# Performance work log

Measured on AMD Instinct MI355X. Metric: run time of the kernel, lower is better.

## Reference

```python
import jax, jax.numpy as jnp
import numpy as np

N = 50000      # nodes
E = 1600000    # edges (avg degree 32)
C_IN = 128
C_H = 128
C_OUT = 10
G = 512        # number of graphs in the batch


def setup_inputs() -> dict:
    key = jax.random.key(0)
    ks = jax.random.split(key, 16)
    x = jax.random.normal(ks[0], (N, C_IN), dtype=jnp.float32)
    edge_index = jax.random.randint(ks[1], (2, E), 0, N, dtype=jnp.int64)
    batch = jnp.sort(jax.random.randint(ks[2], (N,), 0, G, dtype=jnp.int64))

    def lin(k, fan_in, fan_out):
        lim = 1.0 / np.sqrt(fan_in)
        return jax.random.uniform(k, (fan_in, fan_out), jnp.float32, -lim, lim)

    return {
        "x": x, "edge_index": edge_index, "batch": batch,
        # conv1: c_in -> c_hidden
        "Wr1": lin(ks[3], C_IN, C_H), "br1": jnp.zeros((C_H,), jnp.float32),
        "Wo1": lin(ks[4], C_IN, C_H),
        # conv2: c_hidden -> 2*c_hidden
        "Wr2": lin(ks[5], C_H, 2 * C_H), "br2": jnp.zeros((2 * C_H,), jnp.float32),
        "Wo2": lin(ks[6], C_H, 2 * C_H),
        # conv3: 2*c_hidden -> c_hidden
        "Wr3": lin(ks[7], 2 * C_H, C_H), "br3": jnp.zeros((C_H,), jnp.float32),
        "Wo3": lin(ks[8], 2 * C_H, C_H),
        # head
        "W1": lin(ks[9], C_H, 4 * C_OUT), "b1": jnp.zeros((4 * C_OUT,), jnp.float32),
        "W2": lin(ks[10], 4 * C_OUT, C_OUT), "b2": jnp.zeros((C_OUT,), jnp.float32),
    }


def _graph_conv(x, src, dst, Wr, br, Wo):
    # PyG GraphConv: lin_rel(sum_{j in N(i)} x_j) + lin_root(x_i)
    agg = jax.ops.segment_sum(x[src], dst, num_segments=N)  # [N, F_in]
    return agg @ Wr + br + x @ Wo


def reference(x, edge_index, batch, Wr1, br1, Wo1, Wr2, br2, Wo2,
              Wr3, br3, Wo3, W1, b1, W2, b2):
    src, dst = edge_index[0], edge_index[1]
    h = jax.nn.relu(_graph_conv(x, src, dst, Wr1, br1, Wo1))
    h = jax.nn.relu(_graph_conv(h, src, dst, Wr2, br2, Wo2))
    h = _graph_conv(h, src, dst, Wr3, br3, Wo3)
    # global mean pool over graphs
    sums = jax.ops.segment_sum(h, batch, num_segments=G)            # [G, C_H]
    cnts = jax.ops.segment_sum(jnp.ones((N,), h.dtype), batch, num_segments=G)
    pooled = sums / jnp.maximum(cnts, 1.0)[:, None]
    # dropout is identity in eval mode
    out = pooled @ W1 + b1
    out = out @ W2 + b2
    return out
```

## Files before the change

kernel.cpp:

```cpp
#include <hip/hip_runtime.h>
#include <hip/hip_bf16.h>
#include <cstddef>

#define NN 50000
#define EE 1600000
#define GG 512
#define NB 196
#define BSTRIDE 16384
#define BCAP 10240
#define XBLKS 6250
#define SCBLKS 782
#define PSEG 8

typedef unsigned int u32;
typedef unsigned short u16;
typedef __attribute__((ext_vector_type(8))) short frag_ab;
typedef __attribute__((ext_vector_type(4))) float frag_cd;

__device__ __forceinline__ void gl_lds16(const void* g, void* l) {
    __builtin_amdgcn_global_load_lds(
        (const __attribute__((address_space(1))) u32*)g,
        (__attribute__((address_space(3))) u32*)l, 16, 0, 0);
}
__device__ __forceinline__ float b2f_lo(u32 v) { return __uint_as_float(v << 16); }
__device__ __forceinline__ float b2f_hi(u32 v) { return __uint_as_float(v & 0xffff0000u); }
__device__ __forceinline__ float b2f(u32 v, int odd) { return odd ? b2f_hi(v) : b2f_lo(v); }
__device__ __forceinline__ u16 f2b(float x) {
    __hip_bfloat16 h = __float2bfloat16(x);
    return *(u16*)&h;
}
__device__ __forceinline__ u32 pack2(float lo, float hi) {
    return ((u32)f2b(hi) << 16) | f2b(lo);
}
__device__ __forceinline__ void acc2(float2& a, u32 v) {
    a.x += b2f_lo(v);
    a.y += b2f_hi(v);
}

__device__ inline int lower_bound_i(const int* a, int n, int v) {
    int lo = 0, hi = n;
    while (lo < hi) {
        int m = (lo + hi) >> 1;
        if (a[m] < v) lo = m + 1; else hi = m;
    }
    return lo;
}



__global__ __launch_bounds__(256) void bscatter_prep_kernel(
    const int* __restrict__ ei, int* __restrict__ bcnt, u32* __restrict__ pairs,
    const float* __restrict__ x, u16* __restrict__ ax,
    const float* __restrict__ Wr1, const float* __restrict__ Wo1,
    const float* __restrict__ Wr2, const float* __restrict__ Wo2,
    const float* __restrict__ Wr3, const float* __restrict__ Wo3,
    const float* __restrict__ br3,
    u16* __restrict__ BT1, u16* __restrict__ BT2, u16* __restrict__ BT3,
    float* __restrict__ bias3, const int* __restrict__ batch,
    int* __restrict__ gn) {
    __shared__ int lcnt[NB];
    __shared__ int lbase[NB];
    __shared__ unsigned short lpos[2048];
    int bid = blockIdx.x, t = threadIdx.x;
    if (bid < SCBLKS) {
        int e0 = bid * 2048;
        u32 pk[8];
        int bk[8];
        for (int i = t; i < NB; i += 256) lcnt[i] = 0;
        __syncthreads();
#pragma unroll
        for (int i = 0; i < 8; ++i) {
            int e = e0 + i * 256 + t;
            if (e < EE) {
                int dst = ei[EE + e], src = ei[e];
                int b = dst >> 8;
                bk[i] = b;
                pk[i] = ((u32)src << 8) | (u32)(dst & 255);
                lpos[i * 256 + t] = (unsigned short)atomicAdd(&lcnt[b], 1);
            } else bk[i] = -1;
        }
        __syncthreads();
        for (int i = t; i < NB; i += 256) lbase[i] = atomicAdd(&bcnt[i], lcnt[i]);
        __syncthreads();
#pragma unroll
        for (int i = 0; i < 8; ++i) {
            if (bk[i] >= 0) {
                int pos = lbase[bk[i]] + (int)lpos[i * 256 + t];
                pairs[(size_t)bk[i] * BSTRIDE + pos] = pk[i];
            }
        }
    } else if (bid < SCBLKS + XBLKS) {
        int idx = (bid - SCBLKS) * 256 + t;
        int row = idx >> 5, q = idx & 31;
        float4 v = *(const float4*)(x + (size_t)row * 128 + q * 4);
        *(u32*)(ax + (size_t)row * 256 + 128 + q * 4) = pack2(v.x, v.y);
        *(u32*)(ax + (size_t)row * 256 + 128 + q * 4 + 2) = pack2(v.z, v.w);
    } else if (bid < SCBLKS + XBLKS + 256) {
        int m = bid - SCBLKS - XBLKS;
        int k = t;
        BT2[m * 256 + k] = f2b(k < 128 ? Wr2[k * 256 + m] : Wo2[(k - 128) * 256 + m]);
        BT3[m * 256 + k] = f2b(m < 128 ? Wr3[k * 128 + m] : Wo3[k * 128 + (m - 128)]);
        if (m < 128)
            BT1[m * 256 + k] = f2b(k < 128 ? Wr1[k * 128 + m] : Wo1[(k - 128) * 128 + m]);
        if (k == 0) bias3[m] = (m < 128) ? 0.f : br3[m - 128];
    } else {
        int g = (bid - SCBLKS - XBLKS - 256) * 256 + t;
        if (g <= GG) gn[g] = lower_bound_i(batch, NN, g);
    }
}


__global__ __launch_bounds__(512) void bfill_kernel(const u32* __restrict__ pairs,
                                                    const int* __restrict__ bcnt,
                                                    int* __restrict__ ofs,
                                                    u16* __restrict__ srcl) {
    __shared__ int sc[256];
    __shared__ int cnts[256];
    __shared__ int lcnt[256];
    __shared__ int lcur[256];
    __shared__ int lbuf[BCAP];
    int b = blockIdx.x, t = threadIdx.x;
    if (t < 256) {
        int c = (t < NB) ? bcnt[t] : 0;
        cnts[t] = c;
        sc[t] = c;
        lcnt[t] = 0;
    }
    __syncthreads();
    for (int off = 1; off < 256; off <<= 1) {
        int v = (t >= off && t < 256) ? sc[t - off] : 0;
        __syncthreads();
        if (t < 256) sc[t] += v;
        __syncthreads();
    }
    int base = sc[b] - cnts[b];
    int span = cnts[b];
    const u32* pp = pairs + (size_t)b * BSTRIDE;
    for (int j = t; j < span; j += 512) atomicAdd(&lcnt[pp[j] & 255u], 1);
    __syncthreads();
    int nc = 0;
    if (t < 256) {
        nc = lcnt[t];
        sc[t] = nc;
    }
    __syncthreads();
    for (int off = 1; off < 256; off <<= 1) {
        int v = (t >= off && t < 256) ? sc[t - off] : 0;
        __syncthreads();
        if (t < 256) sc[t] += v;
        __syncthreads();
    }
    if (t < 256) {
        int excl = sc[t] - nc;
        int node = b * 256 + t;
        if (node < NN) ofs[node] = base + excl;
        lcur[t] = excl;
    }
    if (b == 0 && t == 256) ofs[NN] = EE;
    __syncthreads();
    for (int j = t; j < span; j += 512) {
        u32 p = pp[j];
        int pos = atomicAdd(&lcur[p & 255u], 1);
        int src = (int)(p >> 8);
        if (pos < BCAP) lbuf[pos] = src;
        else srcl[base + pos] = (u16)src;
    }
    __syncthreads();
    int lim = span < BCAP ? span : BCAP;
    for (int j = t; j < lim; j += 512) srcl[base + j] = (u16)lbuf[j];
}


__global__ __launch_bounds__(256) void pull_bf_kernel(const u32* __restrict__ Xu,
                                                      const int* __restrict__ ofs,
                                                      const u16* __restrict__ srcl,
                                                      u32* __restrict__ outu) {
    int node = (blockIdx.x * 256 + threadIdx.x) >> 6;
    int lane = threadIdx.x & 63;
    int q = lane >> 4, l = lane & 15;
    int lo = ofs[node], hi = ofs[node + 1];
    float2 a0 = {0.f, 0.f}, a1 = {0.f, 0.f}, a2 = {0.f, 0.f}, a3 = {0.f, 0.f};
    int j = lo;
    for (; j + 15 < hi; j += 16) {
        int s0 = srcl[j + q], s1 = srcl[j + 4 + q];
        int s2 = srcl[j + 8 + q], s3 = srcl[j + 12 + q];
        uint4 v0 = *(const uint4*)(Xu + (size_t)s0 * 128 + l * 4);
        uint4 v1 = *(const uint4*)(Xu + (size_t)s1 * 128 + l * 4);
        uint4 v2 = *(const uint4*)(Xu + (size_t)s2 * 128 + l * 4);
        uint4 v3 = *(const uint4*)(Xu + (size_t)s3 * 128 + l * 4);
        acc2(a0, v0.x); acc2(a1, v0.y); acc2(a2, v0.z); acc2(a3, v0.w);
        acc2(a0, v1.x); acc2(a1, v1.y); acc2(a2, v1.z); acc2(a3, v1.w);
        acc2(a0, v2.x); acc2(a1, v2.y); acc2(a2, v2.z); acc2(a3, v2.w);
        acc2(a0, v3.x); acc2(a1, v3.y); acc2(a2, v3.z); acc2(a3, v3.w);
    }
    for (; j + 3 < hi; j += 4) {
        int s = srcl[j + q];
        uint4 v = *(const uint4*)(Xu + (size_t)s * 128 + l * 4);
        acc2(a0, v.x); acc2(a1, v.y); acc2(a2, v.z); acc2(a3, v.w);
    }
    if (j + q < hi) {
        int s = srcl[j + q];
        uint4 v = *(const uint4*)(Xu + (size_t)s * 128 + l * 4);
        acc2(a0, v.x); acc2(a1, v.y); acc2(a2, v.z); acc2(a3, v.w);
    }
    float acc[8] = {a0.x, a0.y, a1.x, a1.y, a2.x, a2.y, a3.x, a3.y};
#pragma unroll
    for (int i = 0; i < 8; ++i) {
        acc[i] += __shfl_xor(acc[i], 16, 64);
        acc[i] += __shfl_xor(acc[i], 32, 64);
    }
    if (q == 0) {
        uint4 r;
        r.x = pack2(acc[0], acc[1]);
        r.y = pack2(acc[2], acc[3]);
        r.z = pack2(acc[4], acc[5]);
        r.w = pack2(acc[6], acc[7]);
        *(uint4*)(outu + (size_t)node * 128 + l * 4) = r;
    }
}


__global__ __launch_bounds__(256, 2) void gemm_bf_kernel(
    const u16* __restrict__ A, const u16* __restrict__ BT,
    const float* __restrict__ bias, u16* __restrict__ C,
    int ldc, int coloff, int relu) {
    __shared__ alignas(16) u16 As[128 * 32];
    __shared__ alignas(16) u16 Bs[128 * 32];
    const int t = threadIdx.x;
    const int lane = t & 63, wid = t >> 6;
    const int quad = lane >> 4, l16 = lane & 15;
    const int wm = wid >> 1, wn = wid & 1;
    const int row0 = blockIdx.y * 128, c0 = blockIdx.x * 128;

    frag_cd acc[4][4];
#pragma unroll
    for (int i = 0; i < 4; ++i)
#pragma unroll
        for (int j = 0; j < 4; ++j) acc[i][j] = (frag_cd)0.f;

    const int ca = t, cb = t + 256;
    const int ra = ca >> 2, oa = (ca & 3) * 8;
    const int rb = cb >> 2, ob = (cb & 3) * 8;
    const int garow = min(row0 + ra, NN - 1);
    const int gbrow = min(row0 + rb, NN - 1);
    const size_t gA1 = (size_t)garow * 256 + oa;
    const size_t gA2 = (size_t)gbrow * 256 + ob;
    const size_t gB1 = (size_t)(c0 + ra) * 256 + oa;
    const size_t gB2 = (size_t)(c0 + rb) * 256 + ob;

    for (int kk = 0; kk < 256; kk += 32) {
        __syncthreads();
        gl_lds16(A + gA1 + kk, &As[ca * 8]);
        gl_lds16(A + gA2 + kk, &As[cb * 8]);
        gl_lds16(BT + gB1 + kk, &Bs[ca * 8]);
        gl_lds16(BT + gB2 + kk, &Bs[cb * 8]);
        __syncthreads();

        frag_ab a[4], b[4];
#pragma unroll
        for (int mt = 0; mt < 4; ++mt)
            a[mt] = *(const frag_ab*)&As[(wm * 64 + mt * 16 + l16) * 32 + quad * 8];
#pragma unroll
        for (int nt = 0; nt < 4; ++nt)
            b[nt] = *(const frag_ab*)&Bs[(wn * 64 + nt * 16 + l16) * 32 + quad * 8];
#pragma unroll
        for (int mt = 0; mt < 4; ++mt)
#pragma unroll
            for (int nt = 0; nt < 4; ++nt)
                acc[mt][nt] = __builtin_amdgcn_mfma_f32_16x16x32_bf16(
                    a[mt], b[nt], acc[mt][nt], 0, 0, 0);
    }

#pragma unroll
    for (int nt = 0; nt < 4; ++nt) {
        int col = c0 + wn * 64 + nt * 16 + l16;
        float bv = bias[col];
#pragma unroll
        for (int mt = 0; mt < 4; ++mt) {
#pragma unroll
            for (int r = 0; r < 4; ++r) {
                int row = row0 + wm * 64 + mt * 16 + quad * 4 + r;
                if (row < NN) {
                    float v = acc[mt][nt][r] + bv;
                    if (relu) v = fmaxf(v, 0.f);
                    C[(size_t)row * ldc + coloff + col] = f2b(v);
                }
            }
        }
    }
}


__global__ __launch_bounds__(256, 2) void gemm23_kernel(
    const u16* __restrict__ A, const u16* __restrict__ BT2,
    const float* __restrict__ br2, const u16* __restrict__ BT3,
    const float* __restrict__ bias3, u16* __restrict__ C) {
    __shared__ alignas(16) u16 As[128 * 32];
    __shared__ alignas(16) u16 Bs[128 * 32];
    __shared__ alignas(16) u16 Hs[128 * 256];
    const int t = threadIdx.x;
    const int lane = t & 63, wid = t >> 6;
    const int quad = lane >> 4, l16 = lane & 15;
    const int wm = wid >> 1, wn = wid & 1;
    const int row0 = blockIdx.x * 128;

    const int ca = t, cb = t + 256;
    const int ra = ca >> 2, oa = (ca & 3) * 8;
    const int rb = cb >> 2, ob = (cb & 3) * 8;
    const int garow = min(row0 + ra, NN - 1);
    const int gbrow = min(row0 + rb, NN - 1);
    const size_t gA1 = (size_t)garow * 256 + oa;
    const size_t gA2 = (size_t)gbrow * 256 + ob;

    for (int nb = 0; nb < 2; ++nb) {
        const int c0 = nb * 128;
        frag_cd acc[4][4];
#pragma unroll
        for (int i = 0; i < 4; ++i)
#pragma unroll
            for (int j = 0; j < 4; ++j) acc[i][j] = (frag_cd)0.f;

        for (int kk = 0; kk < 256; kk += 32) {
            __syncthreads();
            gl_lds16(A + gA1 + kk, &As[ca * 8]);
            gl_lds16(A + gA2 + kk, &As[cb * 8]);
            gl_lds16(BT2 + (size_t)(c0 + ra) * 256 + kk + oa, &Bs[ca * 8]);
            gl_lds16(BT2 + (size_t)(c0 + rb) * 256 + kk + ob, &Bs[cb * 8]);
            __syncthreads();

            frag_ab a[4], b[4];
#pragma unroll
            for (int mt = 0; mt < 4; ++mt)
                a[mt] = *(const frag_ab*)&As[(wm * 64 + mt * 16 + l16) * 32 + quad * 8];
#pragma unroll
            for (int nt = 0; nt < 4; ++nt)
                b[nt] = *(const frag_ab*)&Bs[(wn * 64 + nt * 16 + l16) * 32 + quad * 8];
#pragma unroll
            for (int mt = 0; mt < 4; ++mt)
#pragma unroll
                for (int nt = 0; nt < 4; ++nt)
                    acc[mt][nt] = __builtin_amdgcn_mfma_f32_16x16x32_bf16(
                        a[mt], b[nt], acc[mt][nt], 0, 0, 0);
        }
#pragma unroll
        for (int nt = 0; nt < 4; ++nt) {
            int col = c0 + wn * 64 + nt * 16 + l16;
            float bv = br2[col];
#pragma unroll
            for (int mt = 0; mt < 4; ++mt) {
#pragma unroll
                for (int r = 0; r < 4; ++r) {
                    int lr = wm * 64 + mt * 16 + quad * 4 + r;
                    float v = fmaxf(acc[mt][nt][r] + bv, 0.f);
                    Hs[(lr * 256 + col) ^ ((lr & 7) << 3)] = f2b(v);
                }
            }
        }
    }
    __syncthreads();

    for (int nb = 0; nb < 2; ++nb) {
        const int c0 = nb * 128;
        frag_cd acc[4][4];
#pragma unroll
        for (int i = 0; i < 4; ++i)
#pragma unroll
            for (int j = 0; j < 4; ++j) acc[i][j] = (frag_cd)0.f;

        for (int kk = 0; kk < 256; kk += 32) {
            __syncthreads();
            gl_lds16(BT3 + (size_t)(c0 + ra) * 256 + kk + oa, &Bs[ca * 8]);
            gl_lds16(BT3 + (size_t)(c0 + rb) * 256 + kk + ob, &Bs[cb * 8]);
            __syncthreads();

            frag_ab a[4], b[4];
#pragma unroll
            for (int mt = 0; mt < 4; ++mt) {
                int lr = wm * 64 + mt * 16 + l16;
                a[mt] = *(const frag_ab*)&Hs[(lr * 256 + kk + quad * 8) ^ ((lr & 7) << 3)];
            }
#pragma unroll
            for (int nt = 0; nt < 4; ++nt)
                b[nt] = *(const frag_ab*)&Bs[(wn * 64 + nt * 16 + l16) * 32 + quad * 8];
#pragma unroll
            for (int mt = 0; mt < 4; ++mt)
#pragma unroll
                for (int nt = 0; nt < 4; ++nt)
                    acc[mt][nt] = __builtin_amdgcn_mfma_f32_16x16x32_bf16(
                        a[mt], b[nt], acc[mt][nt], 0, 0, 0);
        }
#pragma unroll
        for (int nt = 0; nt < 4; ++nt) {
            int col = c0 + wn * 64 + nt * 16 + l16;
            float bv = bias3[col];
#pragma unroll
            for (int mt = 0; mt < 4; ++mt) {
#pragma unroll
                for (int r = 0; r < 4; ++r) {
                    int row = row0 + wm * 64 + mt * 16 + quad * 4 + r;
                    if (row < NN) {
                        float v = acc[mt][nt][r] + bv;
                        C[(size_t)row * 256 + col] = f2b(v);
                    }
                }
            }
        }
    }
}


__global__ __launch_bounds__(256) void pool3_seg_kernel(
    const u32* __restrict__ Tu, const int* __restrict__ ofs,
    const u16* __restrict__ srcl, const int* __restrict__ gn,
    float* __restrict__ psum) {
    __shared__ float red[4][128];
    __shared__ float po[2][128];
    int gb = blockIdx.x;
    int g = gb >> 3, s = gb & 7;
    int t = threadIdx.x;
    int w = t >> 6, lane = t & 63;
    int q = lane >> 4, l = lane & 15;
    int n_lo = gn[g], n_hi = gn[g + 1];
    int glo = ofs[n_lo], ghi = ofs[n_hi];
    int len = ghi - glo;
    int s_lo = glo + (int)(((long long)len * s) >> 3);
    int s_hi = glo + (int)(((long long)len * (s + 1)) >> 3);
    int slen = s_hi - s_lo;
    int wlo = s_lo + ((slen * w) >> 2);
    int whi = s_lo + ((slen * (w + 1)) >> 2);

    float2 a0 = {0.f, 0.f}, a1 = {0.f, 0.f}, a2 = {0.f, 0.f}, a3 = {0.f, 0.f};
    int j = wlo;
    for (; j + 15 < whi; j += 16) {
        int s0 = srcl[j + q], s1 = srcl[j + 4 + q];
        int s2 = srcl[j + 8 + q], s3 = srcl[j + 12 + q];
        uint4 v0 = *(const uint4*)(Tu + (size_t)s0 * 128 + l * 4);
        uint4 v1 = *(const uint4*)(Tu + (size_t)s1 * 128 + l * 4);
        uint4 v2 = *(const uint4*)(Tu + (size_t)s2 * 128 + l * 4);
        uint4 v3 = *(const uint4*)(Tu + (size_t)s3 * 128 + l * 4);
        acc2(a0, v0.x); acc2(a1, v0.y); acc2(a2, v0.z); acc2(a3, v0.w);
        acc2(a0, v1.x); acc2(a1, v1.y); acc2(a2, v1.z); acc2(a3, v1.w);
        acc2(a0, v2.x); acc2(a1, v2.y); acc2(a2, v2.z); acc2(a3, v2.w);
        acc2(a0, v3.x); acc2(a1, v3.y); acc2(a2, v3.z); acc2(a3, v3.w);
    }
    for (; j + 3 < whi; j += 4) {
        int sv = srcl[j + q];
        uint4 v = *(const uint4*)(Tu + (size_t)sv * 128 + l * 4);
        acc2(a0, v.x); acc2(a1, v.y); acc2(a2, v.z); acc2(a3, v.w);
    }
    if (j + q < whi) {
        int sv = srcl[j + q];
        uint4 v = *(const uint4*)(Tu + (size_t)sv * 128 + l * 4);
        acc2(a0, v.x); acc2(a1, v.y); acc2(a2, v.z); acc2(a3, v.w);
    }
    float acc[8] = {a0.x, a0.y, a1.x, a1.y, a2.x, a2.y, a3.x, a3.y};
#pragma unroll
    for (int i = 0; i < 8; ++i) {
        acc[i] += __shfl_xor(acc[i], 16, 64);
        acc[i] += __shfl_xor(acc[i], 32, 64);
    }
    if (q == 0) {
#pragma unroll
        for (int i = 0; i < 8; ++i) red[w][l * 8 + i] = acc[i];
    }
    float so = 0.f;
    int ch = t & 127, rg = t >> 7;
    for (int r = n_lo + s * 2 + rg; r < n_hi; r += 16)
        so += b2f(Tu[(size_t)r * 128 + 64 + (ch >> 1)], ch & 1);
    po[rg][ch] = so;
    __syncthreads();
    if (t < 128) {
        float v = red[0][t] + red[1][t] + red[2][t] + red[3][t] + po[0][t] + po[1][t];
        psum[((size_t)g * PSEG + s) * 128 + t] = v;
    }
}


__global__ __launch_bounds__(128) void head_kernel(
    const float* __restrict__ psum, const int* __restrict__ gn,
    const float* __restrict__ W1, const float* __restrict__ b1,
    const float* __restrict__ W2, const float* __restrict__ b2,
    float* __restrict__ out) {
    __shared__ float p[128];
    __shared__ float hid[40];
    int g = blockIdx.x, t = threadIdx.x;
    int cnt = gn[g + 1] - gn[g];
    float sv = 0.f;
#pragma unroll
    for (int k = 0; k < PSEG; ++k) sv += psum[((size_t)g * PSEG + k) * 128 + t];
    p[t] = sv / fmaxf((float)cnt, 1.f);
    __syncthreads();
    if (t < 40) {
        float v = b1[t];
        for (int k = 0; k < 128; ++k) v += p[k] * W1[k * 40 + t];
        hid[t] = v;
    }
    __syncthreads();
    if (t < 10) {
        float v = b2[t];
        for (int j = 0; j < 40; ++j) v += hid[j] * W2[j * 10 + t];
        out[g * 10 + t] = v;
    }
}


extern "C" void kernel_launch(void* const* d_in, const int* in_sizes, int n_in,
                              void* d_out, int out_size, void* d_ws, size_t ws_size,
                              hipStream_t stream) {
    const float* x   = (const float*)d_in[0];
    const int* ei    = (const int*)d_in[1];
    const int* batch = (const int*)d_in[2];
    const float* Wr1 = (const float*)d_in[3];
    const float* br1 = (const float*)d_in[4];
    const float* Wo1 = (const float*)d_in[5];
    const float* Wr2 = (const float*)d_in[6];
    const float* br2 = (const float*)d_in[7];
    const float* Wo2 = (const float*)d_in[8];
    const float* Wr3 = (const float*)d_in[9];
    const float* br3 = (const float*)d_in[10];
    const float* Wo3 = (const float*)d_in[11];
    const float* W1  = (const float*)d_in[12];
    const float* b1  = (const float*)d_in[13];
    const float* W2  = (const float*)d_in[14];
    const float* b2  = (const float*)d_in[15];
    float* out = (float*)d_out;

    char* ws = (char*)d_ws;
    size_t off = 0;
    auto alloc = [&](size_t bytes) {
        void* p = ws + off;
        off += (bytes + 255) & ~(size_t)255;
        return p;
    };
    int* ofs      = (int*)alloc((NN + 1) * sizeof(int));
    int* bcnt     = (int*)alloc(256 * sizeof(int));
    int* gn       = (int*)alloc((GG + 1) * sizeof(int));
    u16* srcl     = (u16*)alloc((size_t)EE * 2);
    u16* ax       = (u16*)alloc((size_t)NN * 256 * 2);
    u16* ah1      = (u16*)alloc((size_t)NN * 256 * 2);
    u16* t3o3     = (u16*)alloc((size_t)NN * 256 * 2);
    float* psum   = (float*)alloc((size_t)GG * PSEG * 128 * sizeof(float));
    u16* BT1      = (u16*)alloc(128 * 256 * 2);
    u16* BT2      = (u16*)alloc(256 * 256 * 2);
    u16* BT3      = (u16*)alloc(256 * 256 * 2);
    float* bias3  = (float*)alloc(256 * sizeof(float));
    u32* pairs = (u32*)t3o3;

    hipMemsetAsync(bcnt, 0, 256 * sizeof(int), stream);

    bscatter_prep_kernel<<<SCBLKS + XBLKS + 256 + 3, 256, 0, stream>>>(
        ei, bcnt, pairs, x, ax, Wr1, Wo1, Wr2, Wo2, Wr3, Wo3, br3,
        BT1, BT2, BT3, bias3, batch, gn);
    bfill_kernel<<<NB, 512, 0, stream>>>(pairs, bcnt, ofs, srcl);

    pull_bf_kernel<<<NN * 64 / 256, 256, 0, stream>>>((const u32*)ax + 64, ofs, srcl, (u32*)ax);
    gemm_bf_kernel<<<dim3(1, 391), 256, 0, stream>>>(ax, BT1, br1, ah1, 256, 128, 1);
    pull_bf_kernel<<<NN * 64 / 256, 256, 0, stream>>>((const u32*)ah1 + 64, ofs, srcl, (u32*)ah1);
    gemm23_kernel<<<391, 256, 0, stream>>>(ah1, BT2, br2, BT3, bias3, t3o3);

    pool3_seg_kernel<<<GG * PSEG, 256, 0, stream>>>((const u32*)t3o3, ofs, srcl, gn, psum);
    head_kernel<<<GG, 128, 0, stream>>>(psum, gn, W1, b1, W2, b2, out);
}
```

Before: 344.2 us.

## Load GEMM fragments directly from global, merge N-blocks, stage output through LDS

The fused conv2/conv3 GEMM kernel no longer stages A and B tiles through LDS with per-k barriers. Each wave now loads MFMA fragments straight from global memory and computes both 128-column halves in one K loop, doubling the accumulator registers. The final output is written into the swizzled Hs buffer and then copied out with coalesced 16-byte stores. The aim is to drop the barriers and LDS round trips, at the cost of more register pressure (occupancy risk under launch_bounds 256,2) and uncoalesced, possibly redundant global fragment loads.

```diff
diff --git a/kernel.cpp b/kernel.cpp
--- a/kernel.cpp
+++ b/kernel.cpp
@@ -295,8 +295,6 @@
     const u16* __restrict__ A, const u16* __restrict__ BT2,
     const float* __restrict__ br2, const u16* __restrict__ BT3,
     const float* __restrict__ bias3, u16* __restrict__ C) {
-    __shared__ alignas(16) u16 As[128 * 32];
-    __shared__ alignas(16) u16 Bs[128 * 32];
     __shared__ alignas(16) u16 Hs[128 * 256];
     const int t = threadIdx.x;
     const int lane = t & 63, wid = t >> 6;
@@ -304,107 +302,118 @@
     const int wm = wid >> 1, wn = wid & 1;
     const int row0 = blockIdx.x * 128;
 
-    const int ca = t, cb = t + 256;
-    const int ra = ca >> 2, oa = (ca & 3) * 8;
-    const int rb = cb >> 2, ob = (cb & 3) * 8;
-    const int garow = min(row0 + ra, NN - 1);
-    const int gbrow = min(row0 + rb, NN - 1);
-    const size_t gA1 = (size_t)garow * 256 + oa;
-    const size_t gA2 = (size_t)gbrow * 256 + ob;
-
-    for (int nb = 0; nb < 2; ++nb) {
-        const int c0 = nb * 128;
-        frag_cd acc[4][4];
+    size_t aoff[4];
+#pragma unroll
+    for (int mt = 0; mt < 4; ++mt) {
+        int r = min(row0 + wm * 64 + mt * 16 + l16, NN - 1);
+        aoff[mt] = (size_t)r * 256 + quad * 8;
+    }
+    size_t boff[2][4];
+#pragma unroll
+    for (int nb = 0; nb < 2; ++nb)
+#pragma unroll
+        for (int nt = 0; nt < 4; ++nt)
+            boff[nb][nt] = (size_t)(nb * 128 + wn * 64 + nt * 16 + l16) * 256 + quad * 8;
+
+    frag_cd acc[2][4][4];
+#pragma unroll
+    for (int nb = 0; nb < 2; ++nb)
 #pragma unroll
         for (int i = 0; i < 4; ++i)
 #pragma unroll
-            for (int j = 0; j < 4; ++j) acc[i][j] = (frag_cd)0.f;
-
-        for (int kk = 0; kk < 256; kk += 32) {
-            __syncthreads();
-            gl_lds16(A + gA1 + kk, &As[ca * 8]);
-            gl_lds16(A + gA2 + kk, &As[cb * 8]);
-            gl_lds16(BT2 + (size_t)(c0 + ra) * 256 + kk + oa, &Bs[ca * 8]);
-            gl_lds16(BT2 + (size_t)(c0 + rb) * 256 + kk + ob, &Bs[cb * 8]);
-            __syncthreads();
-
-            frag_ab a[4], b[4];
+            for (int j = 0; j < 4; ++j) acc[nb][i][j] = (frag_cd)0.f;
+
+    for (int kk = 0; kk < 256; kk += 32) {
+        frag_ab a[4], b[2][4];
+#pragma unroll
+        for (int mt = 0; mt < 4; ++mt)
+            a[mt] = *(const frag_ab*)(A + aoff[mt] + kk);
+#pragma unroll
+        for (int nb = 0; nb < 2; ++nb)
+#pragma unroll
+            for (int nt = 0; nt < 4; ++nt)
+                b[nb][nt] = *(const frag_ab*)(BT2 + boff[nb][nt] + kk);
+#pragma unroll
+        for (int nb = 0; nb < 2; ++nb)
 #pragma unroll
             for (int mt = 0; mt < 4; ++mt)
-                a[mt] = *(const frag_ab*)&As[(wm * 64 + mt * 16 + l16) * 32 + quad * 8];
-#pragma unroll
-            for (int nt = 0; nt < 4; ++nt)
-                b[nt] = *(const frag_ab*)&Bs[(wn * 64 + nt * 16 + l16) * 32 + quad * 8];
+#pragma unroll
+                for (int nt = 0; nt < 4; ++nt)
+                    acc[nb][mt][nt] = __builtin_amdgcn_mfma_f32_16x16x32_bf16(
+                        a[mt], b[nb][nt], acc[nb][mt][nt], 0, 0, 0);
+    }
+#pragma unroll
+    for (int nb = 0; nb < 2; ++nb)
+#pragma unroll
+        for (int nt = 0; nt < 4; ++nt) {
+            int col = nb * 128 + wn * 64 + nt * 16 + l16;
+            float bv = br2[col];
 #pragma unroll
             for (int mt = 0; mt < 4; ++mt)
-#pragma unroll
-                for (int nt = 0; nt < 4; ++nt)
-                    acc[mt][nt] = __builtin_amdgcn_mfma_f32_16x16x32_bf16(
-                        a[mt], b[nt], acc[mt][nt], 0, 0, 0);
-        }
-#pragma unroll
-        for (int nt = 0; nt < 4; ++nt) {
-            int col = c0 + wn * 64 + nt * 16 + l16;
-            float bv = br2[col];
-#pragma unroll
-            for (int mt = 0; mt < 4; ++mt) {
 #pragma unroll
                 for (int r = 0; r < 4; ++r) {
                     int lr = wm * 64 + mt * 16 + quad * 4 + r;
-                    float v = fmaxf(acc[mt][nt][r] + bv, 0.f);
+                    float v = fmaxf(acc[nb][mt][nt][r] + bv, 0.f);
                     Hs[(lr * 256 + col) ^ ((lr & 7) << 3)] = f2b(v);
                 }
-            }
         }
-    }
-    __syncthreads();
-
-    for (int nb = 0; nb < 2; ++nb) {
-        const int c0 = nb * 128;
-        frag_cd acc[4][4];
+    __syncthreads();
+
+    int hrow[4];
+#pragma unroll
+    for (int mt = 0; mt < 4; ++mt) hrow[mt] = wm * 64 + mt * 16 + l16;
+#pragma unroll
+    for (int nb = 0; nb < 2; ++nb)
 #pragma unroll
         for (int i = 0; i < 4; ++i)
 #pragma unroll
-            for (int j = 0; j < 4; ++j) acc[i][j] = (frag_cd)0.f;
-
-        for (int kk = 0; kk < 256; kk += 32) {
-            __syncthreads();
-            gl_lds16(BT3 + (size_t)(c0 + ra) * 256 + kk + oa, &Bs[ca * 8]);
-            gl_lds16(BT3 + (size_t)(c0 + rb) * 256 + kk + ob, &Bs[cb * 8]);
-            __syncthreads();
-
-            frag_ab a[4], b[4];
-#pragma unroll
-            for (int mt = 0; mt < 4; ++mt) {
-                int lr = wm * 64 + mt * 16 + l16;
-                a[mt] = *(const frag_ab*)&Hs[(lr * 256 + kk + quad * 8) ^ ((lr & 7) << 3)];
-            }
+            for (int j = 0; j < 4; ++j) acc[nb][i][j] = (frag_cd)0.f;
+    for (int kk = 0; kk < 256; kk += 32) {
+        frag_ab a[4], b[2][4];
+#pragma unroll
+        for (int mt = 0; mt < 4; ++mt)
+            a[mt] = *(const frag_ab*)&Hs[(hrow[mt] * 256 + kk + quad * 8) ^
+                                         ((hrow[mt] & 7) << 3)];
+#pragma unroll
+        for (int nb = 0; nb < 2; ++nb)
 #pragma unroll
             for (int nt = 0; nt < 4; ++nt)
-                b[nt] = *(const frag_ab*)&Bs[(wn * 64 + nt * 16 + l16) * 32 + quad * 8];
+                b[nb][nt] = *(const frag_ab*)(BT3 + boff[nb][nt] + kk);
+#pragma unroll
+        for (int nb = 0; nb < 2; ++nb)
 #pragma unroll
             for (int mt = 0; mt < 4; ++mt)
 #pragma unroll
                 for (int nt = 0; nt < 4; ++nt)
-                    acc[mt][nt] = __builtin_amdgcn_mfma_f32_16x16x32_bf16(
-                        a[mt], b[nt], acc[mt][nt], 0, 0, 0);
+                    acc[nb][mt][nt] = __builtin_amdgcn_mfma_f32_16x16x32_bf16(
+                        a[mt], b[nb][nt], acc[nb][mt][nt], 0, 0, 0);
+    }
+    __syncthreads();
+
+#pragma unroll
+    for (int nb = 0; nb < 2; ++nb)
+#pragma unroll
+        for (int nt = 0; nt < 4; ++nt) {
+            int col = nb * 128 + wn * 64 + nt * 16 + l16;
+            float bv = bias3[col];
+#pragma unroll
+            for (int mt = 0; mt < 4; ++mt)
+#pragma unroll
+                for (int r = 0; r < 4; ++r) {
+                    int lr = wm * 64 + mt * 16 + quad * 4 + r;
+                    Hs[(lr * 256 + col) ^ ((lr & 7) << 3)] = f2b(acc[nb][mt][nt][r] + bv);
+                }
         }
-#pragma unroll
-        for (int nt = 0; nt < 4; ++nt) {
-            int col = c0 + wn * 64 + nt * 16 + l16;
-            float bv = bias3[col];
-#pragma unroll
-            for (int mt = 0; mt < 4; ++mt) {
-#pragma unroll
-                for (int r = 0; r < 4; ++r) {
-                    int row = row0 + wm * 64 + mt * 16 + quad * 4 + r;
-                    if (row < NN) {
-                        float v = acc[mt][nt][r] + bv;
-                        C[(size_t)row * 256 + col] = f2b(v);
-                    }
-                }
-            }
-        }
+    __syncthreads();
+    const uint4* Hs128 = (const uint4*)Hs;
+#pragma unroll
+    for (int it = 0; it < 16; ++it) {
+        int row = it * 8 + (t >> 5);
+        int grp = t & 31;
+        uint4 v = Hs128[row * 32 + (grp ^ (row & 7))];
+        int grow = row0 + row;
+        if (grow < NN)
+            *(uint4*)(C + (size_t)grow * 256 + grp * 8) = v;
     }
 }
 
```

New measurement: 375.3 us. 9.1% more time.

## Retile fused conv2/conv3 GEMM to 64-row blocks with full-width N and staged stores

Applied to the files above, without the earlier changes.

The fused gemm23 kernel now works on 64-row tiles with each wave computing a full 16x256 strip, instead of 128-row tiles split 2x2 across waves with two N passes. The grid doubles to 782 blocks and LDS use shrinks, so launch bounds rise to 3 blocks per CU. The output is written back through the swizzled LDS buffer as coalesced 16-byte stores instead of scattered 2-byte stores. The intent is more parallelism across CUs and better write coalescing. The cost is that B tiles are reloaded per 64 rows, which doubles weight traffic, and 16 accumulators per wave add register pressure.

```diff
diff --git a/kernel.cpp b/kernel.cpp
--- a/kernel.cpp
+++ b/kernel.cpp
@@ -291,120 +291,96 @@
 }
 
 
-__global__ __launch_bounds__(256, 2) void gemm23_kernel(
+__global__ __launch_bounds__(256, 3) void gemm23_kernel(
     const u16* __restrict__ A, const u16* __restrict__ BT2,
     const float* __restrict__ br2, const u16* __restrict__ BT3,
     const float* __restrict__ bias3, u16* __restrict__ C) {
-    __shared__ alignas(16) u16 As[128 * 32];
-    __shared__ alignas(16) u16 Bs[128 * 32];
-    __shared__ alignas(16) u16 Hs[128 * 256];
+    __shared__ alignas(16) u16 As[64 * 32];
+    __shared__ alignas(16) u16 Bs[256 * 32];
+    __shared__ alignas(16) u16 Hs[64 * 256];
     const int t = threadIdx.x;
-    const int lane = t & 63, wid = t >> 6;
+    const int lane = t & 63, w = t >> 6;
     const int quad = lane >> 4, l16 = lane & 15;
-    const int wm = wid >> 1, wn = wid & 1;
-    const int row0 = blockIdx.x * 128;
-
-    const int ca = t, cb = t + 256;
-    const int ra = ca >> 2, oa = (ca & 3) * 8;
-    const int rb = cb >> 2, ob = (cb & 3) * 8;
+    const int row0 = blockIdx.x * 64;
+
+    const int ra = t >> 2, oa = (t & 3) * 8;
     const int garow = min(row0 + ra, NN - 1);
-    const int gbrow = min(row0 + rb, NN - 1);
-    const size_t gA1 = (size_t)garow * 256 + oa;
-    const size_t gA2 = (size_t)gbrow * 256 + ob;
-
-    for (int nb = 0; nb < 2; ++nb) {
-        const int c0 = nb * 128;
-        frag_cd acc[4][4];
+    const size_t gA = (size_t)garow * 256 + oa;
+    size_t gB[4];
+#pragma unroll
+    for (int i = 0; i < 4; ++i) {
+        int cbi = i * 256 + t;
+        gB[i] = (size_t)(cbi >> 2) * 256 + (cbi & 3) * 8;
+    }
+
+    frag_cd acc[16];
+#pragma unroll
+    for (int i = 0; i < 16; ++i) acc[i] = (frag_cd)0.f;
+
+    for (int kk = 0; kk < 256; kk += 32) {
+        __syncthreads();
+        gl_lds16(A + gA + kk, &As[t * 8]);
 #pragma unroll
         for (int i = 0; i < 4; ++i)
-#pragma unroll
-            for (int j = 0; j < 4; ++j) acc[i][j] = (frag_cd)0.f;
-
-        for (int kk = 0; kk < 256; kk += 32) {
-            __syncthreads();
-            gl_lds16(A + gA1 + kk, &As[ca * 8]);
-            gl_lds16(A + gA2 + kk, &As[cb * 8]);
-            gl_lds16(BT2 + (size_t)(c0 + ra) * 256 + kk + oa, &Bs[ca * 8]);
-            gl_lds16(BT2 + (size_t)(c0 + rb) * 256 + kk + ob, &Bs[cb * 8]);
-            __syncthreads();
-
-            frag_ab a[4], b[4];
-#pragma unroll
-            for (int mt = 0; mt < 4; ++mt)
-                a[mt] = *(const frag_ab*)&As[(wm * 64 + mt * 16 + l16) * 32 + quad * 8];
-#pragma unroll
-            for (int nt = 0; nt < 4; ++nt)
-                b[nt] = *(const frag_ab*)&Bs[(wn * 64 + nt * 16 + l16) * 32 + quad * 8];
-#pragma unroll
-            for (int mt = 0; mt < 4; ++mt)
-#pragma unroll
-                for (int nt = 0; nt < 4; ++nt)
-                    acc[mt][nt] = __builtin_amdgcn_mfma_f32_16x16x32_bf16(
-                        a[mt], b[nt], acc[mt][nt], 0, 0, 0);
-        }
-#pragma unroll
-        for (int nt = 0; nt < 4; ++nt) {
-            int col = c0 + wn * 64 + nt * 16 + l16;
-            float bv = br2[col];
-#pragma unroll
-            for (int mt = 0; mt < 4; ++mt) {
-#pragma unroll
-                for (int r = 0; r < 4; ++r) {
-                    int lr = wm * 64 + mt * 16 + quad * 4 + r;
-                    float v = fmaxf(acc[mt][nt][r] + bv, 0.f);
-                    Hs[(lr * 256 + col) ^ ((lr & 7) << 3)] = f2b(v);
-                }
-            }
-        }
-    }
-    __syncthreads();
-
-    for (int nb = 0; nb < 2; ++nb) {
-        const int c0 = nb * 128;
-        frag_cd acc[4][4];
+            gl_lds16(BT2 + gB[i] + kk, &Bs[(i * 256 + t) * 8]);
+        __syncthreads();
+        frag_ab a = *(const frag_ab*)&As[(w * 16 + l16) * 32 + quad * 8];
+#pragma unroll
+        for (int nt = 0; nt < 16; ++nt) {
+            frag_ab b = *(const frag_ab*)&Bs[(nt * 16 + l16) * 32 + quad * 8];
+            acc[nt] = __builtin_amdgcn_mfma_f32_16x16x32_bf16(a, b, acc[nt], 0, 0, 0);
+        }
+    }
+#pragma unroll
+    for (int nt = 0; nt < 16; ++nt) {
+        int col = nt * 16 + l16;
+        float bv = br2[col];
+#pragma unroll
+        for (int r = 0; r < 4; ++r) {
+            int lr = w * 16 + quad * 4 + r;
+            float v = fmaxf(acc[nt][r] + bv, 0.f);
+            Hs[(lr * 256 + col) ^ ((lr & 7) << 3)] = f2b(v);
+        }
+    }
+
+#pragma unroll
+    for (int i = 0; i < 16; ++i) acc[i] = (frag_cd)0.f;
+    const int hrow = w * 16 + l16;
+    for (int kk = 0; kk < 256; kk += 32) {
+        __syncthreads();
 #pragma unroll
         for (int i = 0; i < 4; ++i)
-#pragma unroll
-            for (int j = 0; j < 4; ++j) acc[i][j] = (frag_cd)0.f;
-
-        for (int kk = 0; kk < 256; kk += 32) {
-            __syncthreads();
-            gl_lds16(BT3 + (size_t)(c0 + ra) * 256 + kk + oa, &Bs[ca * 8]);
-            gl_lds16(BT3 + (size_t)(c0 + rb) * 256 + kk + ob, &Bs[cb * 8]);
-            __syncthreads();
-
-            frag_ab a[4], b[4];
-#pragma unroll
-            for (int mt = 0; mt < 4; ++mt) {
-                int lr = wm * 64 + mt * 16 + l16;
-                a[mt] = *(const frag_ab*)&Hs[(lr * 256 + kk + quad * 8) ^ ((lr & 7) << 3)];
-            }
-#pragma unroll
-            for (int nt = 0; nt < 4; ++nt)
-                b[nt] = *(const frag_ab*)&Bs[(wn * 64 + nt * 16 + l16) * 32 + quad * 8];
-#pragma unroll
-            for (int mt = 0; mt < 4; ++mt)
-#pragma unroll
-                for (int nt = 0; nt < 4; ++nt)
-                    acc[mt][nt] = __builtin_amdgcn_mfma_f32_16x16x32_bf16(
-                        a[mt], b[nt], acc[mt][nt], 0, 0, 0);
-        }
-#pragma unroll
-        for (int nt = 0; nt < 4; ++nt) {
-            int col = c0 + wn * 64 + nt * 16 + l16;
-            float bv = bias3[col];
-#pragma unroll
-            for (int mt = 0; mt < 4; ++mt) {
-#pragma unroll
-                for (int r = 0; r < 4; ++r) {
-                    int row = row0 + wm * 64 + mt * 16 + quad * 4 + r;
-                    if (row < NN) {
-                        float v = acc[mt][nt][r] + bv;
-                        C[(size_t)row * 256 + col] = f2b(v);
-                    }
-                }
-            }
-        }
+            gl_lds16(BT3 + gB[i] + kk, &Bs[(i * 256 + t) * 8]);
+        __syncthreads();
+        frag_ab a = *(const frag_ab*)&Hs[(hrow * 256 + kk + quad * 8) ^
+                                         ((hrow & 7) << 3)];
+#pragma unroll
+        for (int nt = 0; nt < 16; ++nt) {
+            frag_ab b = *(const frag_ab*)&Bs[(nt * 16 + l16) * 32 + quad * 8];
+            acc[nt] = __builtin_amdgcn_mfma_f32_16x16x32_bf16(a, b, acc[nt], 0, 0, 0);
+        }
+    }
+
+#pragma unroll
+    for (int nt = 0; nt < 16; ++nt) {
+        int col = nt * 16 + l16;
+        float bv = bias3[col];
+#pragma unroll
+        for (int r = 0; r < 4; ++r) {
+            int lr = w * 16 + quad * 4 + r;
+            Hs[(lr * 256 + col) ^ ((lr & 7) << 3)] = f2b(acc[nt][r] + bv);
+        }
+    }
+    __syncthreads();
+    const uint4* Hs128 = (const uint4*)Hs;
+#pragma unroll
+    for (int it = 0; it < 8; ++it) {
+        int row = it * 8 + (t >> 5);
+        int grp = t & 31;
+        uint4 v = Hs128[row * 32 + (grp ^ (row & 7))];
+        int grow = row0 + row;
+        if (grow < NN)
+            *(uint4*)(C + (size_t)grow * 256 + grp * 8) = v;
     }
 }
 
@@ -556,7 +532,7 @@
     pull_bf_kernel<<<NN * 64 / 256, 256, 0, stream>>>((const u32*)ax + 64, ofs, srcl, (u32*)ax);
     gemm_bf_kernel<<<dim3(1, 391), 256, 0, stream>>>(ax, BT1, br1, ah1, 256, 128, 1);
     pull_bf_kernel<<<NN * 64 / 256, 256, 0, stream>>>((const u32*)ah1 + 64, ofs, srcl, (u32*)ah1);
-    gemm23_kernel<<<391, 256, 0, stream>>>(ah1, BT2, br2, BT3, bias3, t3o3);
+    gemm23_kernel<<<782, 256, 0, stream>>>(ah1, BT2, br2, BT3, bias3, t3o3);
 
     pool3_seg_kernel<<<GG * PSEG, 256, 0, stream>>>((const u32*)t3o3, ofs, srcl, gn, psum);
     head_kernel<<<GG, 128, 0, stream>>>(psum, gn, W1, b1, W2, b2, out);
```

After: 340.0 us. Within noise of the previous version (-1.2%).
